# Kernel tuning notes

Measured on AMD Instinct MI355X. Metric: run time of the kernel, lower is better.

## Reference

```python
import jax, jax.numpy as jnp
import numpy as np

DIM = 512
WIN = 8
HEADS = 16
HEAD_DIM = DIM // HEADS
N = WIN * WIN
B_ = 1568


def _rel_pos_idx(window_size: int) -> np.ndarray:
    ch = np.arange(window_size)
    cw = np.arange(window_size)
    coords = np.stack(np.meshgrid(ch, cw, indexing='ij'))  # [2, W, W]
    flat = coords.reshape(2, -1)                            # [2, N]
    rel = flat[:, :, None] - flat[:, None, :]               # [2, N, N]
    rel = rel.transpose(1, 2, 0).copy()                     # [N, N, 2]
    rel[:, :, 0] += window_size - 1
    rel[:, :, 1] += window_size - 1
    rel[:, :, 0] *= 2 * window_size - 1
    return rel.sum(-1).astype(np.int32)                     # [N, N]


def setup_inputs() -> dict:
    key = jax.random.key(0)
    kx, kt, kq, kp, kb = jax.random.split(key, 5)
    x = jax.random.normal(kx, (B_, N, DIM), dtype=jnp.float32)
    # learned params
    table = jax.random.normal(kt, ((2 * WIN - 1) ** 2, HEADS), dtype=jnp.float32) * 0.02
    qkv_w = jax.random.normal(kq, (3 * DIM, DIM), dtype=jnp.float32) * (1.0 / np.sqrt(DIM))
    proj_w = jax.random.normal(kp, (DIM, DIM), dtype=jnp.float32) * (1.0 / np.sqrt(DIM))
    proj_b = jax.random.normal(kb, (DIM,), dtype=jnp.float32) * 0.02
    rel_idx = jnp.asarray(_rel_pos_idx(WIN))  # [N, N] int32
    return {"x": x, "qkv_w": qkv_w, "table": table, "proj_w": proj_w,
            "proj_b": proj_b, "rel_idx": rel_idx}


def reference(x, qkv_w, table, proj_w, proj_b, rel_idx):
    Bw, n, c = x.shape
    scale = jnp.sqrt(jnp.float32(HEAD_DIM))
    # qkv: Linear no-bias, torch weight [3C, C] -> x @ W^T
    qkv = (x @ qkv_w.T).reshape(Bw, n, 3, HEADS, HEAD_DIM)
    qkv = jnp.transpose(qkv, (2, 0, 3, 1, 4))  # [3, B, H, N, hd]
    q, k, v = qkv[0], qkv[1], qkv[2]
    attn = jnp.einsum('bhnd,bhmd->bhnm', q, k) / scale  # [B, H, N, N]
    bias = table[rel_idx]                                # [N, N, H]
    attn = attn + jnp.transpose(bias, (2, 0, 1))[None]   # [B, H, N, N]
    attn = jax.nn.softmax(attn, axis=-1)
    out = jnp.einsum('bhnm,bhmd->bhnd', attn, v)         # [B, H, N, hd]
    out = jnp.transpose(out, (0, 2, 1, 3)).reshape(Bw, n, c)
    return out @ proj_w.T + proj_b
```

## Files before the change

### kernel.cpp

```cpp
#include <hip/hip_runtime.h>
#include <stdint.h>

typedef unsigned short ushort_t;
typedef unsigned long long u64_t;
typedef __attribute__((ext_vector_type(4))) float f32x4;
typedef __attribute__((ext_vector_type(8))) short s16x8;

#define S1_ELEMS ((size_t)1568*64*512)

__device__ __forceinline__ ushort_t f2bf(float f) {
  unsigned u = __builtin_bit_cast(unsigned, f);
  u = u + 0x7fffu + ((u >> 16) & 1u);
  return (ushort_t)(u >> 16);
}

__device__ __forceinline__ void gl_lds16(const ushort_t* g, ushort_t* l) {
  typedef __attribute__((address_space(1))) void gvoid;
  typedef __attribute__((address_space(3))) void lvoid;
  __builtin_amdgcn_global_load_lds((gvoid*)(ushort_t*)g, (lvoid*)l, 16, 0, 0);
}

__global__ void k_convert_hi(const float* __restrict__ src, ushort_t* __restrict__ hi, long n8) {
  long i = (long)blockIdx.x * blockDim.x + threadIdx.x;
  long stride = (long)gridDim.x * blockDim.x;
  for (; i < n8; i += stride) {
    float4 v0 = ((const float4*)src)[2*i];
    float4 v1 = ((const float4*)src)[2*i + 1];
    s16x8 pk;
    pk[0] = (short)f2bf(v0.x); pk[1] = (short)f2bf(v0.y);
    pk[2] = (short)f2bf(v0.z); pk[3] = (short)f2bf(v0.w);
    pk[4] = (short)f2bf(v1.x); pk[5] = (short)f2bf(v1.y);
    pk[6] = (short)f2bf(v1.z); pk[7] = (short)f2bf(v1.w);
    *(s16x8*)&hi[i*8] = pk;
  }
}

__global__ void k_bias(const float* __restrict__ table, const int* __restrict__ rel_idx,
                       float* __restrict__ bias) {
  int i = blockIdx.x * 256 + threadIdx.x;
  int h = i >> 12, rc = i & 4095;
  bias[i] = table[rel_idx[rc] * 16 + h];
}

__device__ __forceinline__ void gemm256_loop(
    ushort_t* lds, const ushort_t* pA, const ushort_t* pB,
    int w, int lane, int wm, int wn, f32x4 (&acc)[8][4]) {
  #pragma unroll
  for (int q = 0; q < 2; q++) {
    gl_lds16(pA + q*8192 +  0, lds + ((2*w + q)*2 + 0)*512);
    gl_lds16(pA + q*8192 + 32, lds + ((2*w + q)*2 + 1)*512);
    gl_lds16(pB + q*8192 +  0, lds + 16384 + ((2*w + q)*2 + 0)*512);
    gl_lds16(pB + q*8192 + 32, lds + 16384 + ((2*w + q)*2 + 1)*512);
  }
  asm volatile("s_waitcnt vmcnt(0)" ::: "memory");
  __builtin_amdgcn_s_barrier();

  for (int tau = 0; tau < 8; ++tau) {
    ushort_t* bufR = lds + (tau & 1)*32768;
    ushort_t* bufW = lds + ((tau & 1) ^ 1)*32768;
    if (tau < 7) {
      int ko = (tau + 1)*64;
      #pragma unroll
      for (int q = 0; q < 2; q++) {
        gl_lds16(pA + q*8192 + ko,      bufW + ((2*w + q)*2 + 0)*512);
        gl_lds16(pA + q*8192 + ko + 32, bufW + ((2*w + q)*2 + 1)*512);
        gl_lds16(pB + q*8192 + ko,      bufW + 16384 + ((2*w + q)*2 + 0)*512);
        gl_lds16(pB + q*8192 + ko + 32, bufW + 16384 + ((2*w + q)*2 + 1)*512);
      }
    }
    s16x8 af[4][2], bf[4][2];
    #pragma unroll
    for (int t = 0; t < 4; t++)
      #pragma unroll
      for (int kh = 0; kh < 2; kh++) {
        af[t][kh] = *(const s16x8*)&bufR[((wm*8 + t)*2 + kh)*512 + lane*8];
        bf[t][kh] = *(const s16x8*)&bufR[16384 + ((wn*4 + t)*2 + kh)*512 + lane*8];
      }
    __builtin_amdgcn_s_barrier();
    asm volatile("s_waitcnt lgkmcnt(0)" ::: "memory");
    __builtin_amdgcn_sched_barrier(0);
    __builtin_amdgcn_s_setprio(1);
    #pragma unroll
    for (int t = 0; t < 4; t++)
      #pragma unroll
      for (int tb = 0; tb < 4; tb++) {
        acc[t][tb] = __builtin_amdgcn_mfma_f32_16x16x32_bf16(af[t][0], bf[tb][0], acc[t][tb], 0, 0, 0);
        acc[t][tb] = __builtin_amdgcn_mfma_f32_16x16x32_bf16(af[t][1], bf[tb][1], acc[t][tb], 0, 0, 0);
      }
    __builtin_amdgcn_s_setprio(0);
    s16x8 ag[4][2];
    #pragma unroll
    for (int t = 0; t < 4; t++)
      #pragma unroll
      for (int kh = 0; kh < 2; kh++)
        ag[t][kh] = *(const s16x8*)&bufR[((wm*8 + 4 + t)*2 + kh)*512 + lane*8];
    asm volatile("s_waitcnt lgkmcnt(0)" ::: "memory");
    __builtin_amdgcn_sched_barrier(0);
    __builtin_amdgcn_s_setprio(1);
    #pragma unroll
    for (int t = 0; t < 4; t++)
      #pragma unroll
      for (int tb = 0; tb < 4; tb++) {
        acc[4 + t][tb] = __builtin_amdgcn_mfma_f32_16x16x32_bf16(ag[t][0], bf[tb][0], acc[4 + t][tb], 0, 0, 0);
        acc[4 + t][tb] = __builtin_amdgcn_mfma_f32_16x16x32_bf16(ag[t][1], bf[tb][1], acc[4 + t][tb], 0, 0, 0);
      }
    __builtin_amdgcn_s_setprio(0);
    asm volatile("s_waitcnt vmcnt(0)" ::: "memory");
    __builtin_amdgcn_s_barrier();
  }
}

__global__ __launch_bounds__(512, 2) void k_gemm_qkv(
    const ushort_t* __restrict__ xh, const ushort_t* __restrict__ wh,
    ushort_t* __restrict__ qh, ushort_t* __restrict__ kh, ushort_t* __restrict__ vt) {
  extern __shared__ __align__(16) ushort_t lds[];
  const int tid = threadIdx.x, w = tid >> 6, lane = tid & 63;
  const int g = lane >> 4, l15 = lane & 15;
  const int wm = w >> 2, wn = w & 3;
  int flat = blockIdx.x;
  int swz = (flat & 7) * 294 + (flat >> 3);
  int bx = swz % 6, by = swz / 6;

  const ushort_t* pA = xh + ((size_t)by*256 + (size_t)(32*w) + l15)*512 + g*8;
  const ushort_t* pB = wh + ((size_t)bx*256 + (size_t)(32*w) + l15)*512 + g*8;

  f32x4 acc[8][4];
  #pragma unroll
  for (int r = 0; r < 8; r++)
    #pragma unroll
    for (int c = 0; c < 4; c++) acc[r][c] = (f32x4){0.f, 0.f, 0.f, 0.f};

  gemm256_loop(lds, pA, pB, w, lane, wm, wn, acc);

  asm volatile("" ::: "memory");
  const int sel = bx >> 1;
  if (sel < 2) {
    #pragma unroll
    for (int ra = 0; ra < 8; ra++)
      #pragma unroll
      for (int tb = 0; tb < 4; tb++)
        #pragma unroll
        for (int j = 0; j < 4; j++) {
          int row = wm*128 + ra*16 + g*4 + j;
          int col = wn*64 + tb*16 + l15;
          int r = (row >> 6)*8 + (col >> 5);
          int n = row & 63, d = col & 31;
          int byte = r*4096 + ((n*64 + d*2) ^ ((n & 12) << 3));
          *(ushort_t*)((char*)lds + byte) = f2bf(acc[ra][tb][j]);
        }
  } else {
    #pragma unroll
    for (int ra = 0; ra < 8; ra++)
      #pragma unroll
      for (int tb = 0; tb < 4; tb++) {
        int row0 = wm*128 + ra*16 + g*4;
        int col = wn*64 + tb*16 + l15;
        int r = (row0 >> 6)*8 + (col >> 5);
        int n0 = row0 & 63, d = col & 31;
        u64_t pk = (u64_t)f2bf(acc[ra][tb][0])
                 | ((u64_t)f2bf(acc[ra][tb][1]) << 16)
                 | ((u64_t)f2bf(acc[ra][tb][2]) << 32)
                 | ((u64_t)f2bf(acc[ra][tb][3]) << 48);
        int byte = r*4096 + ((d*128 + n0*2) ^ ((d & 7) << 4) ^ (((((d >> 3) ^ (n0 >> 3))) & 1) << 6));
        *(u64_t*)((char*)lds + byte) = pk;
      }
  }
  asm volatile("s_waitcnt lgkmcnt(0)" ::: "memory");
  __builtin_amdgcn_s_barrier();
  ushort_t* dst = (sel == 0) ? qh : (sel == 1) ? kh : vt;
  const int hbase = (bx & 1) * 8;
  #pragma unroll
  for (int it = 0; it < 16; it++) {
    int cg = it*512 + tid;
    int r = cg >> 8, inner = cg & 255;
    int byte;
    if (sel < 2) byte = r*4096 + ((inner*16) ^ (((inner >> 2) & 12) << 3));
    else         byte = r*4096 + ((inner*16) ^ (((inner >> 3) & 7) << 4) ^ ((((inner >> 6) ^ inner) & 1) << 6));
    s16x8 v = *(const s16x8*)((const char*)lds + byte);
    int b = by*4 + (r >> 3), h = hbase + (r & 7);
    *(s16x8*)&dst[(size_t)(b*16 + h)*2048 + inner*8] = v;
  }
}

__global__ __launch_bounds__(512, 2) void k_gemm_proj(
    const ushort_t* __restrict__ ah, const ushort_t* __restrict__ wh,
    const float* __restrict__ pb, float* __restrict__ out) {
  extern __shared__ __align__(16) ushort_t lds[];
  const int tid = threadIdx.x, w = tid >> 6, lane = tid & 63;
  const int g = lane >> 4, l15 = lane & 15;
  const int wm = w >> 2, wn = w & 3;
  int flat = blockIdx.x;
  int swz = (flat & 7) * 98 + (flat >> 3);
  int bx = swz & 1, by = swz >> 1;

  const ushort_t* pA = ah + ((size_t)by*256 + (size_t)(2*w)*16 + l15)*512 + g*8;
  const ushort_t* pB = wh + ((size_t)bx*256 + (size_t)(2*w)*16 + l15)*512 + g*8;

  f32x4 acc[8][4];
  #pragma unroll
  for (int r = 0; r < 8; r++)
    #pragma unroll
    for (int c = 0; c < 4; c++) acc[r][c] = (f32x4){0.f, 0.f, 0.f, 0.f};

  gemm256_loop(lds, pA, pB, w, lane, wm, wn, acc);

  asm volatile("" ::: "memory");
  #pragma unroll
  for (int p = 0; p < 2; p++) {
    if (p) { asm volatile("" ::: "memory"); __builtin_amdgcn_s_barrier(); }
    if (wm == p) {
      #pragma unroll
      for (int ra = 0; ra < 8; ra++)
        #pragma unroll
        for (int tb = 0; tb < 4; tb++)
          #pragma unroll
          for (int j = 0; j < 4; j++) {
            int row = ra*16 + g*4 + j;
            int col = wn*64 + tb*16 + l15;
            int byte = (row*1024 + col*4) ^ ((row & 12) << 2) ^ ((row & 8) << 3);
            *(float*)((char*)lds + byte) = acc[ra][tb][j];
          }
    }
    asm volatile("s_waitcnt lgkmcnt(0)" ::: "memory");
    __builtin_amdgcn_s_barrier();
    #pragma unroll
    for (int it = 0; it < 16; it++) {
      int cg = it*512 + tid;
      int row = cg >> 6, c16 = cg & 63;
      int byte = row*1024 + ((c16*16) ^ ((row & 12) << 2) ^ ((row & 8) << 3));
      f32x4 v = *(const f32x4*)((const char*)lds + byte);
      int ncol = bx*256 + c16*4;
      f32x4 pbv = *(const f32x4*)&pb[ncol];
      v = v + pbv;
      *(f32x4*)&out[(size_t)(by*256 + p*128 + row)*512 + ncol] = v;
    }
  }
}

__global__ __launch_bounds__(256) void k_attn(
    const ushort_t* __restrict__ qh, const ushort_t* __restrict__ kh,
    const ushort_t* __restrict__ vt, const float* __restrict__ bias,
    ushort_t* __restrict__ aoh) {
  __shared__ ushort_t plds[4][64*72];
  __shared__ float blds[64*68];
  const int tid = threadIdx.x, w = tid >> 6, lane = tid & 63;
  const int g = lane >> 4, l15 = lane & 15;
  const int h = blockIdx.x & 15;
  const int b = (blockIdx.x >> 4)*4 + w;
  const size_t base = (size_t)(b*16 + h) * 2048;

  const float* bh_ = bias + ((size_t)h << 12);
  #pragma unroll
  for (int it = 0; it < 4; it++) {
    int idx = it*1024 + tid*4;
    int rr = idx >> 6, cc = idx & 63;
    *(f32x4*)&blds[rr*68 + cc] = *(const f32x4*)&bh_[idx];
  }
  __syncthreads();

  s16x8 qf[4], kf[4];
  #pragma unroll
  for (int t = 0; t < 4; t++) {
    size_t o = base + (size_t)(t*16 + l15)*32 + g*8;
    qf[t] = *(const s16x8*)&qh[o];
    kf[t] = *(const s16x8*)&kh[o];
  }
  s16x8 vf[2][2];
  #pragma unroll
  for (int kt = 0; kt < 2; kt++)
    #pragma unroll
    for (int nt = 0; nt < 2; nt++)
      vf[kt][nt] = *(const s16x8*)&vt[base + (size_t)(nt*16 + l15)*64 + kt*32 + g*8];

  f32x4 s[4][4];
  #pragma unroll
  for (int r = 0; r < 4; r++)
    #pragma unroll
    for (int c = 0; c < 4; c++) s[r][c] = (f32x4){0.f,0.f,0.f,0.f};
  #pragma unroll
  for (int r = 0; r < 4; r++)
    #pragma unroll
    for (int c = 0; c < 4; c++)
      s[r][c] = __builtin_amdgcn_mfma_f32_16x16x32_bf16(qf[r], kf[c], s[r][c], 0, 0, 0);

  const float invs = 0.17677669529663687f;
  #pragma unroll
  for (int r = 0; r < 4; r++)
    #pragma unroll
    for (int c = 0; c < 4; c++)
      #pragma unroll
      for (int j = 0; j < 4; j++) {
        int rr = r*16 + g*4 + j, cc = c*16 + l15;
        s[r][c][j] = s[r][c][j]*invs + blds[rr*68 + cc];
      }

  #pragma unroll
  for (int r = 0; r < 4; r++)
    #pragma unroll
    for (int j = 0; j < 4; j++) {
      float mx = fmaxf(fmaxf(s[r][0][j], s[r][1][j]), fmaxf(s[r][2][j], s[r][3][j]));
      mx = fmaxf(mx, __shfl_xor(mx, 1));
      mx = fmaxf(mx, __shfl_xor(mx, 2));
      mx = fmaxf(mx, __shfl_xor(mx, 4));
      mx = fmaxf(mx, __shfl_xor(mx, 8));
      float p0 = __expf(s[r][0][j]-mx), p1 = __expf(s[r][1][j]-mx);
      float p2 = __expf(s[r][2][j]-mx), p3 = __expf(s[r][3][j]-mx);
      float sum = p0 + p1 + p2 + p3;
      sum += __shfl_xor(sum, 1);
      sum += __shfl_xor(sum, 2);
      sum += __shfl_xor(sum, 4);
      sum += __shfl_xor(sum, 8);
      float rv = 1.0f / sum;
      s[r][0][j] = p0*rv; s[r][1][j] = p1*rv; s[r][2][j] = p2*rv; s[r][3][j] = p3*rv;
    }

  ushort_t* Pm = plds[w];
  #pragma unroll
  for (int r = 0; r < 4; r++)
    #pragma unroll
    for (int c = 0; c < 4; c++)
      #pragma unroll
      for (int j = 0; j < 4; j++) {
        int rr = r*16 + g*4 + j, cc = c*16 + l15;
        Pm[rr*72 + cc] = f2bf(s[r][c][j]);
      }
  s16x8 pf[4][2];
  #pragma unroll
  for (int ta = 0; ta < 4; ta++)
    #pragma unroll
    for (int kt = 0; kt < 2; kt++)
      pf[ta][kt] = *(const s16x8*)&Pm[(ta*16 + l15)*72 + kt*32 + g*8];

  f32x4 o[4][2];
  #pragma unroll
  for (int ta = 0; ta < 4; ta++)
    #pragma unroll
    for (int nt = 0; nt < 2; nt++) o[ta][nt] = (f32x4){0.f,0.f,0.f,0.f};
  #pragma unroll
  for (int ta = 0; ta < 4; ta++)
    #pragma unroll
    for (int nt = 0; nt < 2; nt++)
      #pragma unroll
      for (int kt = 0; kt < 2; kt++)
        o[ta][nt] = __builtin_amdgcn_mfma_f32_16x16x32_bf16(pf[ta][kt], vf[kt][nt], o[ta][nt], 0, 0, 0);

  #pragma unroll
  for (int ta = 0; ta < 4; ta++)
    #pragma unroll
    for (int nt = 0; nt < 2; nt++)
      #pragma unroll
      for (int j = 0; j < 4; j++) {
        int rr = ta*16 + g*4 + j, dd = nt*16 + l15;
        aoh[((size_t)b*64 + rr)*512 + h*32 + dd] = f2bf(o[ta][nt][j]);
      }
}

extern "C" void kernel_launch(void* const* d_in, const int* in_sizes, int n_in,
                              void* d_out, int out_size, void* d_ws, size_t ws_size,
                              hipStream_t stream) {
  const float* x      = (const float*)d_in[0];
  const float* qkv_w  = (const float*)d_in[1];
  const float* table  = (const float*)d_in[2];
  const float* proj_w = (const float*)d_in[3];
  const float* proj_b = (const float*)d_in[4];
  const int*   rel_idx = (const int*)d_in[5];

  const size_t S1 = S1_ELEMS;
  const size_t need = (4*S1 + 786432 + 262144)*sizeof(ushort_t) + 65536*sizeof(float);
  if (ws_size < need) return;

  ushort_t* qh  = (ushort_t*)d_ws;
  ushort_t* kh  = qh + S1;
  ushort_t* vt  = kh + S1;
  ushort_t* xh  = vt + S1;
  ushort_t* wqh = xh + S1;
  ushort_t* wph = wqh + 786432;
  float*    bias = (float*)(wph + 262144);
  ushort_t* aoh = xh;

  hipFuncSetAttribute((const void*)k_gemm_qkv,
                      hipFuncAttributeMaxDynamicSharedMemorySize, 131072);
  hipFuncSetAttribute((const void*)k_gemm_proj,
                      hipFuncAttributeMaxDynamicSharedMemorySize, 131072);

  k_convert_hi<<<3136, 256, 0, stream>>>(x, xh, (long)(S1/8));
  k_convert_hi<<<384, 256, 0, stream>>>(qkv_w, wqh, 98304);
  k_convert_hi<<<128, 256, 0, stream>>>(proj_w, wph, 32768);
  k_bias<<<256, 256, 0, stream>>>(table, rel_idx, bias);
  k_gemm_qkv<<<2352, 512, 131072, stream>>>(xh, wqh, qh, kh, vt);
  k_attn<<<6272, 256, 0, stream>>>(qh, kh, vt, bias, aoh);
  k_gemm_proj<<<784, 512, 131072, stream>>>(aoh, wph, proj_b, (float*)d_out);
}
```

Baseline: 544.3 us.

## Fuse prep kernels, finer-grained pipelined QKV GEMM, hoist attention loads

Merges the three conversion launches and the bias gather into one prep kernel to save launch overhead. Restructures the QKV GEMM main loop into four half-K phases per tile, each issuing part of the next tile's global-to-LDS loads with partial vmcnt waits, so memory traffic overlaps MFMA work more finely. In the attention kernel, the Q/K/V register loads are issued before the bias staging and barrier so their latency overlaps it. The cost is more barriers per K tile and more intricate wait-count bookkeeping, which is fragile if any count is off.

```diff
diff --git a/kernel.cpp b/kernel.cpp
--- a/kernel.cpp
+++ b/kernel.cpp
@@ -20,10 +20,30 @@
   __builtin_amdgcn_global_load_lds((gvoid*)(ushort_t*)g, (lvoid*)l, 16, 0, 0);
 }
 
-__global__ void k_convert_hi(const float* __restrict__ src, ushort_t* __restrict__ hi, long n8) {
-  long i = (long)blockIdx.x * blockDim.x + threadIdx.x;
-  long stride = (long)gridDim.x * blockDim.x;
-  for (; i < n8; i += stride) {
+__global__ void k_prep(const float* __restrict__ x, ushort_t* __restrict__ xh,
+                       const float* __restrict__ wq, ushort_t* __restrict__ wqh,
+                       const float* __restrict__ wp, ushort_t* __restrict__ wph,
+                       const float* __restrict__ table, const int* __restrict__ rel_idx,
+                       float* __restrict__ bias) {
+  int blk = blockIdx.x, tid = threadIdx.x;
+  if (blk < 3136) {
+    long i0 = (long)blk*256 + tid;
+    #pragma unroll
+    for (int rep = 0; rep < 8; rep++) {
+      long i = i0 + (long)rep*802816;
+      float4 v0 = ((const float4*)x)[2*i];
+      float4 v1 = ((const float4*)x)[2*i + 1];
+      s16x8 pk;
+      pk[0] = (short)f2bf(v0.x); pk[1] = (short)f2bf(v0.y);
+      pk[2] = (short)f2bf(v0.z); pk[3] = (short)f2bf(v0.w);
+      pk[4] = (short)f2bf(v1.x); pk[5] = (short)f2bf(v1.y);
+      pk[6] = (short)f2bf(v1.z); pk[7] = (short)f2bf(v1.w);
+      *(s16x8*)&xh[i*8] = pk;
+    }
+  } else if (blk < 3648) {
+    const float* src; ushort_t* dst; long i;
+    if (blk < 3520) { src = wq; dst = wqh; i = (long)(blk - 3136)*256 + tid; }
+    else            { src = wp; dst = wph; i = (long)(blk - 3520)*256 + tid; }
     float4 v0 = ((const float4*)src)[2*i];
     float4 v1 = ((const float4*)src)[2*i + 1];
     s16x8 pk;
@@ -31,83 +51,63 @@
     pk[2] = (short)f2bf(v0.z); pk[3] = (short)f2bf(v0.w);
     pk[4] = (short)f2bf(v1.x); pk[5] = (short)f2bf(v1.y);
     pk[6] = (short)f2bf(v1.z); pk[7] = (short)f2bf(v1.w);
-    *(s16x8*)&hi[i*8] = pk;
-  }
-}
-
-__global__ void k_bias(const float* __restrict__ table, const int* __restrict__ rel_idx,
-                       float* __restrict__ bias) {
-  int i = blockIdx.x * 256 + threadIdx.x;
-  int h = i >> 12, rc = i & 4095;
-  bias[i] = table[rel_idx[rc] * 16 + h];
-}
-
-__device__ __forceinline__ void gemm256_loop(
-    ushort_t* lds, const ushort_t* pA, const ushort_t* pB,
-    int w, int lane, int wm, int wn, f32x4 (&acc)[8][4]) {
-  #pragma unroll
-  for (int q = 0; q < 2; q++) {
-    gl_lds16(pA + q*8192 +  0, lds + ((2*w + q)*2 + 0)*512);
-    gl_lds16(pA + q*8192 + 32, lds + ((2*w + q)*2 + 1)*512);
-    gl_lds16(pB + q*8192 +  0, lds + 16384 + ((2*w + q)*2 + 0)*512);
-    gl_lds16(pB + q*8192 + 32, lds + 16384 + ((2*w + q)*2 + 1)*512);
-  }
-  asm volatile("s_waitcnt vmcnt(0)" ::: "memory");
+    *(s16x8*)&dst[i*8] = pk;
+  } else {
+    int i0 = ((blk - 3648)*256 + tid)*4;
+    #pragma unroll
+    for (int j = 0; j < 4; j++) {
+      int i = i0 + j;
+      int h = i >> 12, rc = i & 4095;
+      bias[i] = table[rel_idx[rc] * 16 + h];
+    }
+  }
+}
+
+struct GemmCtx {
+  ushort_t* lds;
+  const ushort_t *pA0, *pA1, *pB0, *pB1;
+  int w, lane, wm, wn;
+};
+
+template<int BUFP, int KH, int RH, int SSEL, int SBUFP, int SU, int VM>
+__device__ __forceinline__ void phase(const GemmCtx& C, f32x4 (&acc)[8][4], s16x8 (&bf)[4], int stau) {
+  s16x8 af[4];
+  #pragma unroll
+  for (int t = 0; t < 4; t++)
+    af[t] = *(const s16x8*)&C.lds[BUFP*32768 + ((C.wm*8 + RH*4 + t)*2 + KH)*512 + C.lane*8];
+  if constexpr (RH == 0) {
+    #pragma unroll
+    for (int t = 0; t < 4; t++)
+      bf[t] = *(const s16x8*)&C.lds[BUFP*32768 + 16384 + ((C.wn*4 + t)*2 + KH)*512 + C.lane*8];
+  }
+  if constexpr (SSEL == 0) {
+    gl_lds16(C.pA0 + stau*64 + SU*32, C.lds + SBUFP*32768 + (4*C.w + SU)*512);
+    gl_lds16(C.pA1 + stau*64 + SU*32, C.lds + SBUFP*32768 + (4*C.w + 2 + SU)*512);
+  } else if constexpr (SSEL == 1) {
+    gl_lds16(C.pB0 + stau*64 + SU*32, C.lds + SBUFP*32768 + 16384 + (4*C.w + SU)*512);
+    gl_lds16(C.pB1 + stau*64 + SU*32, C.lds + SBUFP*32768 + 16384 + (4*C.w + 2 + SU)*512);
+  }
+  if constexpr (VM == 8) asm volatile("s_waitcnt vmcnt(8)" ::: "memory");
+  else if constexpr (VM == 4) asm volatile("s_waitcnt vmcnt(4)" ::: "memory");
+  else if constexpr (VM == 0) asm volatile("s_waitcnt vmcnt(0)" ::: "memory");
   __builtin_amdgcn_s_barrier();
-
-  for (int tau = 0; tau < 8; ++tau) {
-    ushort_t* bufR = lds + (tau & 1)*32768;
-    ushort_t* bufW = lds + ((tau & 1) ^ 1)*32768;
-    if (tau < 7) {
-      int ko = (tau + 1)*64;
-      #pragma unroll
-      for (int q = 0; q < 2; q++) {
-        gl_lds16(pA + q*8192 + ko,      bufW + ((2*w + q)*2 + 0)*512);
-        gl_lds16(pA + q*8192 + ko + 32, bufW + ((2*w + q)*2 + 1)*512);
-        gl_lds16(pB + q*8192 + ko,      bufW + 16384 + ((2*w + q)*2 + 0)*512);
-        gl_lds16(pB + q*8192 + ko + 32, bufW + 16384 + ((2*w + q)*2 + 1)*512);
-      }
-    }
-    s16x8 af[4][2], bf[4][2];
-    #pragma unroll
-    for (int t = 0; t < 4; t++)
-      #pragma unroll
-      for (int kh = 0; kh < 2; kh++) {
-        af[t][kh] = *(const s16x8*)&bufR[((wm*8 + t)*2 + kh)*512 + lane*8];
-        bf[t][kh] = *(const s16x8*)&bufR[16384 + ((wn*4 + t)*2 + kh)*512 + lane*8];
-      }
-    __builtin_amdgcn_s_barrier();
-    asm volatile("s_waitcnt lgkmcnt(0)" ::: "memory");
-    __builtin_amdgcn_sched_barrier(0);
-    __builtin_amdgcn_s_setprio(1);
-    #pragma unroll
-    for (int t = 0; t < 4; t++)
-      #pragma unroll
-      for (int tb = 0; tb < 4; tb++) {
-        acc[t][tb] = __builtin_amdgcn_mfma_f32_16x16x32_bf16(af[t][0], bf[tb][0], acc[t][tb], 0, 0, 0);
-        acc[t][tb] = __builtin_amdgcn_mfma_f32_16x16x32_bf16(af[t][1], bf[tb][1], acc[t][tb], 0, 0, 0);
-      }
-    __builtin_amdgcn_s_setprio(0);
-    s16x8 ag[4][2];
-    #pragma unroll
-    for (int t = 0; t < 4; t++)
-      #pragma unroll
-      for (int kh = 0; kh < 2; kh++)
-        ag[t][kh] = *(const s16x8*)&bufR[((wm*8 + 4 + t)*2 + kh)*512 + lane*8];
-    asm volatile("s_waitcnt lgkmcnt(0)" ::: "memory");
-    __builtin_amdgcn_sched_barrier(0);
-    __builtin_amdgcn_s_setprio(1);
-    #pragma unroll
-    for (int t = 0; t < 4; t++)
-      #pragma unroll
-      for (int tb = 0; tb < 4; tb++) {
-        acc[4 + t][tb] = __builtin_amdgcn_mfma_f32_16x16x32_bf16(ag[t][0], bf[tb][0], acc[4 + t][tb], 0, 0, 0);
-        acc[4 + t][tb] = __builtin_amdgcn_mfma_f32_16x16x32_bf16(ag[t][1], bf[tb][1], acc[4 + t][tb], 0, 0, 0);
-      }
-    __builtin_amdgcn_s_setprio(0);
-    asm volatile("s_waitcnt vmcnt(0)" ::: "memory");
-    __builtin_amdgcn_s_barrier();
-  }
+  __builtin_amdgcn_s_setprio(1);
+  #pragma unroll
+  for (int ta = 0; ta < 4; ta++)
+    #pragma unroll
+    for (int tb = 0; tb < 4; tb++)
+      acc[RH*4 + ta][tb] = __builtin_amdgcn_mfma_f32_16x16x32_bf16(af[ta], bf[tb], acc[RH*4 + ta][tb], 0, 0, 0);
+  __builtin_amdgcn_s_setprio(0);
+  __builtin_amdgcn_s_barrier();
+}
+
+template<int BUFP, bool S12, bool S34, int VM2, int VM4>
+__device__ __forceinline__ void ktile(const GemmCtx& C, f32x4 (&acc)[8][4], int tau) {
+  s16x8 bf[4];
+  phase<BUFP, 0, 0, S12 ? 0 : -1, BUFP^1, 1, -1 >(C, acc, bf, tau + 1);
+  phase<BUFP, 0, 1, S12 ? 1 : -1, BUFP^1, 1, VM2>(C, acc, bf, tau + 1);
+  phase<BUFP, 1, 0, S34 ? 0 : -1, BUFP,   0, -1 >(C, acc, bf, tau + 2);
+  phase<BUFP, 1, 1, S34 ? 1 : -1, BUFP,   0, VM4>(C, acc, bf, tau + 2);
 }
 
 __global__ __launch_bounds__(512, 2) void k_gemm_qkv(
@@ -121,8 +121,13 @@
   int swz = (flat & 7) * 294 + (flat >> 3);
   int bx = swz % 6, by = swz / 6;
 
-  const ushort_t* pA = xh + ((size_t)by*256 + (size_t)(32*w) + l15)*512 + g*8;
-  const ushort_t* pB = wh + ((size_t)bx*256 + (size_t)(32*w) + l15)*512 + g*8;
+  GemmCtx C;
+  C.lds = lds;
+  C.pA0 = xh + ((size_t)by*256 + (size_t)(2*w)*16 + l15)*512 + g*8;
+  C.pA1 = C.pA0 + 16*512;
+  C.pB0 = wh + ((size_t)bx*256 + (size_t)(2*w)*16 + l15)*512 + g*8;
+  C.pB1 = C.pB0 + 16*512;
+  C.w = w; C.lane = lane; C.wm = wm; C.wn = wn;
 
   f32x4 acc[8][4];
   #pragma unroll
@@ -130,7 +135,27 @@
     #pragma unroll
     for (int c = 0; c < 4; c++) acc[r][c] = (f32x4){0.f, 0.f, 0.f, 0.f};
 
-  gemm256_loop(lds, pA, pB, w, lane, wm, wn, acc);
+  gl_lds16(C.pA0 +  0, lds + (4*w + 0)*512);
+  gl_lds16(C.pA1 +  0, lds + (4*w + 2)*512);
+  gl_lds16(C.pB0 +  0, lds + 16384 + (4*w + 0)*512);
+  gl_lds16(C.pB1 +  0, lds + 16384 + (4*w + 2)*512);
+  gl_lds16(C.pA0 + 32, lds + (4*w + 1)*512);
+  gl_lds16(C.pA1 + 32, lds + (4*w + 3)*512);
+  gl_lds16(C.pB0 + 32, lds + 16384 + (4*w + 1)*512);
+  gl_lds16(C.pB1 + 32, lds + 16384 + (4*w + 3)*512);
+  gl_lds16(C.pA0 + 64, lds + 32768 + (4*w + 0)*512);
+  gl_lds16(C.pA1 + 64, lds + 32768 + (4*w + 2)*512);
+  gl_lds16(C.pB0 + 64, lds + 32768 + 16384 + (4*w + 0)*512);
+  gl_lds16(C.pB1 + 64, lds + 32768 + 16384 + (4*w + 2)*512);
+  asm volatile("s_waitcnt vmcnt(4)" ::: "memory");
+  __builtin_amdgcn_s_barrier();
+
+  for (int kt = 0; kt < 6; kt += 2) {
+    ktile<0, true, true, 8, 8>(C, acc, kt);
+    ktile<1, true, true, 8, 8>(C, acc, kt + 1);
+  }
+  ktile<0, true,  false, 8, 4>(C, acc, 6);
+  ktile<1, false, false, 0, -1>(C, acc, 7);
 
   asm volatile("" ::: "memory");
   const int sel = bx >> 1;
@@ -182,6 +207,74 @@
   }
 }
 
+__device__ __forceinline__ void gemm256_loop(
+    ushort_t* lds, const ushort_t* pA, const ushort_t* pB,
+    int w, int lane, int wm, int wn, f32x4 (&acc)[8][4]) {
+  #pragma unroll
+  for (int q = 0; q < 2; q++) {
+    gl_lds16(pA + q*8192 +  0, lds + ((2*w + q)*2 + 0)*512);
+    gl_lds16(pA + q*8192 + 32, lds + ((2*w + q)*2 + 1)*512);
+    gl_lds16(pB + q*8192 +  0, lds + 16384 + ((2*w + q)*2 + 0)*512);
+    gl_lds16(pB + q*8192 + 32, lds + 16384 + ((2*w + q)*2 + 1)*512);
+  }
+  asm volatile("s_waitcnt vmcnt(0)" ::: "memory");
+  __builtin_amdgcn_s_barrier();
+
+  for (int tau = 0; tau < 8; ++tau) {
+    ushort_t* bufR = lds + (tau & 1)*32768;
+    ushort_t* bufW = lds + ((tau & 1) ^ 1)*32768;
+    if (tau < 7) {
+      int ko = (tau + 1)*64;
+      #pragma unroll
+      for (int q = 0; q < 2; q++) {
+        gl_lds16(pA + q*8192 + ko,      bufW + ((2*w + q)*2 + 0)*512);
+        gl_lds16(pA + q*8192 + ko + 32, bufW + ((2*w + q)*2 + 1)*512);
+        gl_lds16(pB + q*8192 + ko,      bufW + 16384 + ((2*w + q)*2 + 0)*512);
+        gl_lds16(pB + q*8192 + ko + 32, bufW + 16384 + ((2*w + q)*2 + 1)*512);
+      }
+    }
+    s16x8 af[4][2], bf[4][2];
+    #pragma unroll
+    for (int t = 0; t < 4; t++)
+      #pragma unroll
+      for (int kh = 0; kh < 2; kh++) {
+        af[t][kh] = *(const s16x8*)&bufR[((wm*8 + t)*2 + kh)*512 + lane*8];
+        bf[t][kh] = *(const s16x8*)&bufR[16384 + ((wn*4 + t)*2 + kh)*512 + lane*8];
+      }
+    __builtin_amdgcn_s_barrier();
+    asm volatile("s_waitcnt lgkmcnt(0)" ::: "memory");
+    __builtin_amdgcn_sched_barrier(0);
+    __builtin_amdgcn_s_setprio(1);
+    #pragma unroll
+    for (int t = 0; t < 4; t++)
+      #pragma unroll
+      for (int tb = 0; tb < 4; tb++) {
+        acc[t][tb] = __builtin_amdgcn_mfma_f32_16x16x32_bf16(af[t][0], bf[tb][0], acc[t][tb], 0, 0, 0);
+        acc[t][tb] = __builtin_amdgcn_mfma_f32_16x16x32_bf16(af[t][1], bf[tb][1], acc[t][tb], 0, 0, 0);
+      }
+    __builtin_amdgcn_s_setprio(0);
+    s16x8 ag[4][2];
+    #pragma unroll
+    for (int t = 0; t < 4; t++)
+      #pragma unroll
+      for (int kh = 0; kh < 2; kh++)
+        ag[t][kh] = *(const s16x8*)&bufR[((wm*8 + 4 + t)*2 + kh)*512 + lane*8];
+    asm volatile("s_waitcnt lgkmcnt(0)" ::: "memory");
+    __builtin_amdgcn_sched_barrier(0);
+    __builtin_amdgcn_s_setprio(1);
+    #pragma unroll
+    for (int t = 0; t < 4; t++)
+      #pragma unroll
+      for (int tb = 0; tb < 4; tb++) {
+        acc[4 + t][tb] = __builtin_amdgcn_mfma_f32_16x16x32_bf16(ag[t][0], bf[tb][0], acc[4 + t][tb], 0, 0, 0);
+        acc[4 + t][tb] = __builtin_amdgcn_mfma_f32_16x16x32_bf16(ag[t][1], bf[tb][1], acc[4 + t][tb], 0, 0, 0);
+      }
+    __builtin_amdgcn_s_setprio(0);
+    asm volatile("s_waitcnt vmcnt(0)" ::: "memory");
+    __builtin_amdgcn_s_barrier();
+  }
+}
+
 __global__ __launch_bounds__(512, 2) void k_gemm_proj(
     const ushort_t* __restrict__ ah, const ushort_t* __restrict__ wh,
     const float* __restrict__ pb, float* __restrict__ out) {
@@ -249,6 +342,20 @@
   const int b = (blockIdx.x >> 4)*4 + w;
   const size_t base = (size_t)(b*16 + h) * 2048;
 
+  s16x8 qf[4], kf[4];
+  #pragma unroll
+  for (int t = 0; t < 4; t++) {
+    size_t o = base + (size_t)(t*16 + l15)*32 + g*8;
+    qf[t] = *(const s16x8*)&qh[o];
+    kf[t] = *(const s16x8*)&kh[o];
+  }
+  s16x8 vf[2][2];
+  #pragma unroll
+  for (int kt = 0; kt < 2; kt++)
+    #pragma unroll
+    for (int nt = 0; nt < 2; nt++)
+      vf[kt][nt] = *(const s16x8*)&vt[base + (size_t)(nt*16 + l15)*64 + kt*32 + g*8];
+
   const float* bh_ = bias + ((size_t)h << 12);
   #pragma unroll
   for (int it = 0; it < 4; it++) {
@@ -257,20 +364,6 @@
     *(f32x4*)&blds[rr*68 + cc] = *(const f32x4*)&bh_[idx];
   }
   __syncthreads();
-
-  s16x8 qf[4], kf[4];
-  #pragma unroll
-  for (int t = 0; t < 4; t++) {
-    size_t o = base + (size_t)(t*16 + l15)*32 + g*8;
-    qf[t] = *(const s16x8*)&qh[o];
-    kf[t] = *(const s16x8*)&kh[o];
-  }
-  s16x8 vf[2][2];
-  #pragma unroll
-  for (int kt = 0; kt < 2; kt++)
-    #pragma unroll
-    for (int nt = 0; nt < 2; nt++)
-      vf[kt][nt] = *(const s16x8*)&vt[base + (size_t)(nt*16 + l15)*64 + kt*32 + g*8];
 
   f32x4 s[4][4];
   #pragma unroll
@@ -383,10 +476,7 @@
   hipFuncSetAttribute((const void*)k_gemm_proj,
                       hipFuncAttributeMaxDynamicSharedMemorySize, 131072);
 
-  k_convert_hi<<<3136, 256, 0, stream>>>(x, xh, (long)(S1/8));
-  k_convert_hi<<<384, 256, 0, stream>>>(qkv_w, wqh, 98304);
-  k_convert_hi<<<128, 256, 0, stream>>>(proj_w, wph, 32768);
-  k_bias<<<256, 256, 0, stream>>>(table, rel_idx, bias);
+  k_prep<<<3712, 256, 0, stream>>>(x, xh, qkv_w, wqh, proj_w, wph, table, rel_idx, bias);
   k_gemm_qkv<<<2352, 512, 131072, stream>>>(xh, wqh, qh, kh, vt);
   k_attn<<<6272, 256, 0, stream>>>(qh, kh, vt, bias, aoh);
   k_gemm_proj<<<784, 512, 131072, stream>>>(aoh, wph, proj_b, (float*)d_out);
```

After: 513.8 us. 1.06x faster.
